# Kernel tuning notes

Hardware: AMD Instinct MI355X
Metric: run time of the kernel (lower is better)

Reference implementation:

```python
import jax, jax.numpy as jnp
import numpy as np

# ---- constants from __init__ ----
DT = 1.0
NX, NY = 192, 192
SRC_X, SRC_Y = 40, 96
PX = jnp.array([160, 160, 160])
PY = jnp.array([48, 96, 144])
PML_N, PML_P, PML_MAX = 20, 4.0, 3.0
C0, C1 = 1.0, 0.9
H = DT * 2.01 / 1.0  # grid spacing


def make_b():
    """PML damping profile b(x,y), [NX, NY]."""
    v = (PML_MAX * np.linspace(0.0, 1.0, PML_N + 1) ** PML_P).astype(np.float32)
    bx = np.zeros((NX, NY), np.float32)
    bx[: PML_N + 1, :] = v[::-1, None]
    bx[NX - PML_N - 1 :, :] = v[:, None]
    by = np.zeros((NX, NY), np.float32)
    by[:, : PML_N + 1] = v[::-1][None, :]
    by[:, NY - PML_N - 1 :] = v[None, :]
    return jnp.asarray(np.sqrt(bx ** 2 + by ** 2))


def _conv3(img, kern):
    # img [B,1,H,W], kern [1,1,3,3], 'same' padding
    return jax.lax.conv_general_dilated(
        img, kern, (1, 1), ((1, 1), (1, 1)),
        dimension_numbers=("NCHW", "OIHW", "NCHW"))


def _proj(x, eta=0.5, beta=100.0):
    return (jnp.tanh(beta * eta) + jnp.tanh(beta * (x - eta))) / (
        jnp.tanh(beta * eta) + jnp.tanh(beta * (1.0 - eta)))


def setup_inputs() -> dict:
    key = jax.random.key(0)
    k1, k2 = jax.random.split(key)
    x = jax.random.normal(k1, (4, 256), dtype=jnp.float32)  # [batch, T]
    rho = jax.random.uniform(k2, (NX, NY), dtype=jnp.float32)
    # clip_pml_rho(): rho[b != 0] = 0 for binarized model (applied at init)
    rho = jnp.where(make_b() != 0, 0.0, rho)
    return {"x": x, "rho": rho}


def reference(x, rho):
    b = make_b()
    lpf_k = jnp.array([[[[0.0, 0.125, 0.0], [0.125, 0.5, 0.125], [0.0, 0.125, 0.0]]]], jnp.float32)
    lap_k = (H ** -2) * jnp.array([[[[0.0, 1.0, 0.0], [1.0, -4.0, 1.0], [0.0, 1.0, 0.0]]]], jnp.float32)
    A1 = 1.0 / (DT ** -2 + b * 0.5 / DT)
    A2 = 2.0 * DT ** -2
    A3 = DT ** -2 - b * 0.5 / DT

    # binarized wave-speed field c(rho): LPF then tanh projection
    lpf_rho = _conv3(rho[None, None], lpf_k)[0, 0]
    c = C0 + (C1 - C0) * _proj(lpf_rho)
    c2 = c * c

    B = x.shape[0]
    y0 = jnp.zeros((B, NX, NY), x.dtype)

    def step(carry, xi):
        y1, y2 = carry
        lap = _conv3(y1[:, None], lap_k)[:, 0]            # [B,NX,NY]
        y = A1 * (A2 * y1 - A3 * y2 + c2 * lap)
        y = y.at[:, SRC_X, SRC_Y].add(xi)                 # source injection
        return (y, y1), y[:, PX, PY]                      # emit probe values [B,P]

    _, probes = jax.lax.scan(step, (y0, y0), x.T)         # probes [T,B,P]

    # integrate_probe_points: sum |y|^2 over time, normalize per batch
    I = jnp.sum(probes ** 2, axis=0)                      # [B,P]
    return I / jnp.sum(I, axis=1, keepdims=True)
```

## Files before the change

### kernel.cpp

```cpp
#include <hip/hip_runtime.h>
#include <math.h>

#define NXY    192
#define CELLS  (NXY*NXY)
#define NBATCH 4
#define NSTEPS 256
#define TCH    16
#define NCHUNK (NSTEPS/TCH)
#define TPB    512
#define NW     8
#define RPL    5
#define OUTR   6
#define NBLKS  256

#define I_OFF   (16*CELLS)
#define FLG_OFF (I_OFF + 64)

typedef float v2f __attribute__((ext_vector_type(2)));

__device__ __forceinline__ float dpp_up1(float v) {
    int r = __builtin_amdgcn_update_dpp(0, __builtin_bit_cast(int, v),
                                        0x138, 0xf, 0xf, true);
    return __builtin_bit_cast(float, r);
}
__device__ __forceinline__ float dpp_dn1(float v) {
    int r = __builtin_amdgcn_update_dpp(0, __builtin_bit_cast(int, v),
                                        0x130, 0xf, 0xf, true);
    return __builtin_bit_cast(float, r);
}

__device__ __forceinline__ float pml_prof(int i) {
    int t;
    if (i <= 20)            t = 20 - i;
    else if (i >= NXY - 21) t = i - (NXY - 21);
    else                    return 0.0f;
    float u  = (float)t * 0.05f;
    float u2 = u * u;
    return 3.0f * u2 * u2;
}

__global__ __launch_bounds__(TPB, 1)
void wave_k(const float* __restrict__ x, const float* __restrict__ rho,
            float* __restrict__ ws, float* __restrict__ out) {
    int blk = ((blockIdx.x & 7) << 5) | (blockIdx.x >> 3);
    int b  = blk / 64;
    int r_ = blk % 64;
    int bi = r_ >> 1, cj = r_ & 1;
    int I0 = OUTR * bi - 17;
    int J0 = 96 * cj - 16;
    int t  = threadIdx.x;
    int w  = t >> 6;
    int l  = t & 63;
    int row0 = I0 + RPL * w;
    int gj   = J0 + 2 * l;

    int* flags = (int*)(ws + FLG_OFF);
    int drt = bi + (t >> 1) - 3;
    int dfi = b * 64 + drt * 2 + (t & 1);
    bool dvalid = (t < 14) && (drt >= 0) && (drt < 32) &&
                  !(drt == bi && (t & 1) == cj);

    __shared__ v2f hb[2][2][NW + 2][64];
    __shared__ float xs[NSTEPS];
    for (int k = t; k < 2 * 2 * (NW + 2) * 64; k += TPB)
        ((v2f*)hb)[k] = (v2f){0.f, 0.f};
    if (t < NSTEPS) xs[t] = x[b * NSTEPS + t];

    bool cok = (gj >= 0 && gj < NXY);

    v2f Ka[RPL], Qa[RPL];
    {
        v2f rv[RPL + 2];
#pragma unroll
        for (int r = 0; r < RPL + 2; r++) {
            int gi = row0 - 1 + r;
            bool ok = cok && gi >= 0 && gi < NXY;
            rv[r] = ok ? *(const v2f*)(rho + gi * NXY + gj) : (v2f){0.f, 0.f};
        }
        const float IH2 = (float)(1.0 / (2.01 * 2.01));
#pragma unroll
        for (int r = 0; r < RPL; r++) {
            int gi = row0 + r;
            v2f rc = rv[r + 1], ru = rv[r], rd = rv[r + 2];
            float lf = dpp_up1(rc.y);
            float rt = dpp_dn1(rc.x);
            float bx = pml_prof(gi);
            v2f K, Q;
            {
                float lpf = 0.5f * rc.x + 0.125f * ((ru.x + rd.x) + (lf + rc.y));
                float p   = 0.5f * (1.0f + tanhf(100.0f * (lpf - 0.5f)));
                float c   = 1.0f - 0.1f * p;
                float by  = pml_prof(gj);
                float bb  = sqrtf(bx * bx + by * by);
                float a1  = 1.0f / (1.0f + 0.5f * bb);
                K.x = a1 * (c * c * IH2);
                Q.x = 1.0f - 2.0f * a1;
            }
            {
                float lpf = 0.5f * rc.y + 0.125f * ((ru.y + rd.y) + (rc.x + rt));
                float p   = 0.5f * (1.0f + tanhf(100.0f * (lpf - 0.5f)));
                float c   = 1.0f - 0.1f * p;
                float by  = pml_prof(gj + 1);
                float bb  = sqrtf(bx * bx + by * by);
                float a1  = 1.0f / (1.0f + 0.5f * bb);
                K.y = a1 * (c * c * IH2);
                Q.y = 1.0f - 2.0f * a1;
            }
            bool ok = cok && gi >= 0 && gi < NXY;
            Ka[r] = ok ? K : (v2f){0.f, 0.f};
            Qa[r] = ok ? Q : (v2f){0.f, 0.f};
        }
    }

    v2f yc[RPL], yp[RPL];
#pragma unroll
    for (int r = 0; r < RPL; r++) { yc[r] = (v2f){0.f, 0.f}; yp[r] = (v2f){0.f, 0.f}; }

    int sr = 40 - I0, sc = 96 - J0;
    bool wave_src = (sr >= RPL * w) && (sr < RPL * w + RPL);
    int src_rl = sr - RPL * w;
    float srcm = (2 * l == sc) ? 1.f : 0.f;

    int pcl = 2 * l + J0;
    bool wave_prb = (bi == 26) && (w == 4);
    const int prb_rl = 1;
    bool is_prb = (cj == 0) ? (pcl == 48) : (pcl == 96 || pcl == 144);
    float prbm = is_prb ? 1.f : 0.f;
    float pacc = 0.f;

    v2f uph, dnh;
    __syncthreads();

#define ROWC(CUR, PRV, rr_, UP, DN, XSV, YN) do {                              \
    v2f cv = CUR[rr_];                                                         \
    float lf0 = dpp_up1(cv.y);                                                 \
    float rt1 = dpp_dn1(cv.x);                                                 \
    v2f h = (v2f){lf0, rt1} + __builtin_shufflevector(cv, cv, 1, 0);           \
    v2f S = ((UP) + (DN)) + h;                                                 \
    YN = cv + Qa[rr_] * (PRV[rr_] - cv) + Ka[rr_] * (S - 4.0f * cv);           \
    if (wave_src && (rr_) == src_rl) YN.x += srcm * (XSV);                     \
    if (wave_prb && (rr_) == prb_rl) { float q = prbm * YN.x; pacc += q * YN.x; } \
} while (0)

#define STEP(CUR, PRV, PH, SIDX) do {                                          \
    v2f y1, y2, y3, t0, t4;                                                    \
    ROWC(CUR, PRV, 1, CUR[0], CUR[2], xv[SIDX], y1);                           \
    ROWC(CUR, PRV, 2, CUR[1], CUR[3], xv[SIDX], y2);                           \
    ROWC(CUR, PRV, 3, CUR[2], CUR[4], xv[SIDX], y3);                           \
    ROWC(CUR, PRV, 0, uph,    CUR[1], xv[SIDX], t0);                           \
    ROWC(CUR, PRV, 4, CUR[3], dnh,    xv[SIDX], t4);                           \
    hb[PH][0][w + 1][l] = t0;                                                  \
    hb[PH][1][w + 1][l] = t4;                                                  \
    PRV[0] = t0; PRV[1] = y1; PRV[2] = y2; PRV[3] = y3; PRV[4] = t4;           \
    __syncthreads();                                                           \
    uph = hb[PH][1][w][l];                                                     \
    dnh = hb[PH][0][w + 2][l];                                                 \
} while (0)

#pragma unroll 1
    for (int chunk = 0; chunk < NCHUNK; chunk++) {
        float xv[TCH];
#pragma unroll
        for (int i = 0; i < TCH; i++) xv[i] = xs[chunk * TCH + i];

        if (chunk) {
            if (dvalid) {
                while (__hip_atomic_load(&flags[dfi], __ATOMIC_RELAXED,
                                         __HIP_MEMORY_SCOPE_AGENT) < chunk) {}
            }
            __syncthreads();

            int pin = chunk & 1;
            const float* curg = ws + ((pin * 2 + 0) * NBATCH + b) * CELLS;
            const float* prvg = ws + ((pin * 2 + 1) * NBATCH + b) * CELLS;
            int  idxr[RPL];
            bool okr[RPL];
#pragma unroll
            for (int r = 0; r < RPL; r++) {
                int gi = row0 + r;
                okr[r]  = cok && gi >= 0 && gi < NXY;
                idxr[r] = okr[r] ? gi * NXY + gj : 0;
            }
            v2f c0, c1, c2, c3, c4, p0, p1, p2, p3, p4;
            asm volatile(
                "global_load_dwordx2 %0, %10, off sc0 sc1\n\t"
                "global_load_dwordx2 %1, %11, off sc0 sc1\n\t"
                "global_load_dwordx2 %2, %12, off sc0 sc1\n\t"
                "global_load_dwordx2 %3, %13, off sc0 sc1\n\t"
                "global_load_dwordx2 %4, %14, off sc0 sc1\n\t"
                "global_load_dwordx2 %5, %15, off sc0 sc1\n\t"
                "global_load_dwordx2 %6, %16, off sc0 sc1\n\t"
                "global_load_dwordx2 %7, %17, off sc0 sc1\n\t"
                "global_load_dwordx2 %8, %18, off sc0 sc1\n\t"
                "global_load_dwordx2 %9, %19, off sc0 sc1\n\t"
                "s_waitcnt vmcnt(0)"
                : "=&v"(c0), "=&v"(c1), "=&v"(c2), "=&v"(c3), "=&v"(c4),
                  "=&v"(p0), "=&v"(p1), "=&v"(p2), "=&v"(p3), "=&v"(p4)
                : "v"(curg + idxr[0]), "v"(curg + idxr[1]), "v"(curg + idxr[2]),
                  "v"(curg + idxr[3]), "v"(curg + idxr[4]),
                  "v"(prvg + idxr[0]), "v"(prvg + idxr[1]), "v"(prvg + idxr[2]),
                  "v"(prvg + idxr[3]), "v"(prvg + idxr[4])
                : "memory");
            yc[0] = okr[0] ? c0 : (v2f){0.f, 0.f};
            yc[1] = okr[1] ? c1 : (v2f){0.f, 0.f};
            yc[2] = okr[2] ? c2 : (v2f){0.f, 0.f};
            yc[3] = okr[3] ? c3 : (v2f){0.f, 0.f};
            yc[4] = okr[4] ? c4 : (v2f){0.f, 0.f};
            yp[0] = okr[0] ? p0 : (v2f){0.f, 0.f};
            yp[1] = okr[1] ? p1 : (v2f){0.f, 0.f};
            yp[2] = okr[2] ? p2 : (v2f){0.f, 0.f};
            yp[3] = okr[3] ? p3 : (v2f){0.f, 0.f};
            yp[4] = okr[4] ? p4 : (v2f){0.f, 0.f};
        }

        hb[0][0][w + 1][l] = yc[0];
        hb[0][1][w + 1][l] = yc[4];
        __syncthreads();
        uph = hb[0][1][w][l];
        dnh = hb[0][0][w + 2][l];

#pragma unroll
        for (int s2 = 0; s2 < TCH / 2; s2++) {
            STEP(yc, yp, 1, 2 * s2);
            STEP(yp, yc, 0, 2 * s2 + 1);
        }

        if (chunk != NCHUNK - 1) {
            int pout = (chunk & 1) ^ 1;
            float* ncurg = ws + ((pout * 2 + 0) * NBATCH + b) * CELLS;
            float* nprvg = ws + ((pout * 2 + 1) * NBATCH + b) * CELLS;
#pragma unroll
            for (int r = 0; r < RPL; r++) {
                int gi = row0 + r;
                if (gi >= OUTR * bi && gi < OUTR * bi + OUTR && l >= 8 && l < 56) {
                    int idx = gi * NXY + gj;
                    asm volatile(
                        "global_store_dwordx2 %0, %2, off sc0 sc1\n\t"
                        "global_store_dwordx2 %1, %3, off sc0 sc1"
                        :: "v"(ncurg + idx), "v"(nprvg + idx),
                           "v"(yc[r]), "v"(yp[r])
                        : "memory");
                }
            }
        } else {
            if (wave_prb && is_prb) {
                float* ip = ws + I_OFF + b * 3 + (pcl / 48 - 1);
                asm volatile("global_store_dword %0, %1, off sc0 sc1"
                             :: "v"(ip), "v"(pacc) : "memory");
            }
        }

        asm volatile("s_waitcnt vmcnt(0)" ::: "memory");
        __syncthreads();
        if (t == 0) {
            __hip_atomic_store(&flags[blk], chunk + 1, __ATOMIC_RELAXED,
                               __HIP_MEMORY_SCOPE_AGENT);
        }
    }
#undef STEP
#undef ROWC

    if (blk == 0) {
        if (t < 8) {
            int pb = (t >> 1) * 64 + 52 + (t & 1);
            while (__hip_atomic_load(&flags[pb], __ATOMIC_RELAXED,
                                     __HIP_MEMORY_SCOPE_AGENT) < NCHUNK) {}
        }
        __syncthreads();
        if (t < 12) {
            const float* I = ws + I_OFF;
            int bb = t / 3;
            float s = 0.f;
#pragma unroll
            for (int k = 0; k < 3; k++)
                s += __hip_atomic_load(I + 3 * bb + k, __ATOMIC_RELAXED,
                                       __HIP_MEMORY_SCOPE_AGENT);
            float num = __hip_atomic_load(I + t, __ATOMIC_RELAXED,
                                          __HIP_MEMORY_SCOPE_AGENT);
            out[t] = num / s;
        }
    }
}

extern "C" void kernel_launch(void* const* d_in, const int* in_sizes, int n_in,
                              void* d_out, int out_size, void* d_ws, size_t ws_size,
                              hipStream_t stream) {
    const float* x   = (const float*)d_in[0];
    const float* rho = (const float*)d_in[1];
    float* ws  = (float*)d_ws;
    float* outp = (float*)d_out;

    hipMemsetAsync((char*)d_ws + I_OFF * sizeof(float), 0,
                   (64 + NBLKS) * sizeof(float), stream);

    wave_k<<<dim3(NBLKS), dim3(TPB), 0, stream>>>(x, rho, ws, outp);
}
```

Measured before the change: 194.4 us.

## Exchange two-row halos per two time steps to halve block barriers

Each wave now keeps a two-row halo on each side and computes two time steps between LDS halo exchanges. The first step redundantly computes 7 rows and the second produces the 5 owned rows, so only one __syncthreads and halo swap happens per pair of steps. The chunk start loads 9 current and 7 previous rows from global memory instead of 5 each. This cuts barrier and LDS latency on the serial time loop in exchange for about 40% more stencil arithmetic per step and higher register use.

```diff
diff --git a/kernel.cpp b/kernel.cpp
--- a/kernel.cpp
+++ b/kernel.cpp
@@ -7,6 +7,7 @@
 #define NSTEPS 256
 #define TCH    16
 #define NCHUNK (NSTEPS/TCH)
+#define NGRP   (TCH/2)
 #define TPB    512
 #define NW     8
 #define RPL    5
@@ -52,6 +53,7 @@
     int w  = t >> 6;
     int l  = t & 63;
     int row0 = I0 + RPL * w;
+    int wr0  = RPL * w;
     int gj   = J0 + 2 * l;
 
     int* flags = (int*)(ws + FLG_OFF);
@@ -60,28 +62,28 @@
     bool dvalid = (t < 14) && (drt >= 0) && (drt < 32) &&
                   !(drt == bi && (t & 1) == cj);
 
-    __shared__ v2f hb[2][2][NW + 2][64];
+    __shared__ v2f hb[2][4][NW + 2][64];
     __shared__ float xs[NSTEPS];
-    for (int k = t; k < 2 * 2 * (NW + 2) * 64; k += TPB)
+    for (int k = t; k < 2 * 4 * (NW + 2) * 64; k += TPB)
         ((v2f*)hb)[k] = (v2f){0.f, 0.f};
     if (t < NSTEPS) xs[t] = x[b * NSTEPS + t];
 
     bool cok = (gj >= 0 && gj < NXY);
 
-    v2f Ka[RPL], Qa[RPL];
+    v2f Ka[7], Qa[7];
     {
-        v2f rv[RPL + 2];
-#pragma unroll
-        for (int r = 0; r < RPL + 2; r++) {
-            int gi = row0 - 1 + r;
+        v2f rv[9];
+#pragma unroll
+        for (int r = 0; r < 9; r++) {
+            int gi = row0 - 2 + r;
             bool ok = cok && gi >= 0 && gi < NXY;
             rv[r] = ok ? *(const v2f*)(rho + gi * NXY + gj) : (v2f){0.f, 0.f};
         }
         const float IH2 = (float)(1.0 / (2.01 * 2.01));
 #pragma unroll
-        for (int r = 0; r < RPL; r++) {
-            int gi = row0 + r;
-            v2f rc = rv[r + 1], ru = rv[r], rd = rv[r + 2];
+        for (int i = 0; i < 7; i++) {
+            int gi = row0 + i - 1;
+            v2f rc = rv[i + 1], ru = rv[i], rd = rv[i + 2];
             float lf = dpp_up1(rc.y);
             float rt = dpp_dn1(rc.x);
             float bx = pml_prof(gi);
@@ -107,54 +109,37 @@
                 Q.y = 1.0f - 2.0f * a1;
             }
             bool ok = cok && gi >= 0 && gi < NXY;
-            Ka[r] = ok ? K : (v2f){0.f, 0.f};
-            Qa[r] = ok ? Q : (v2f){0.f, 0.f};
+            Ka[i] = ok ? K : (v2f){0.f, 0.f};
+            Qa[i] = ok ? Q : (v2f){0.f, 0.f};
         }
     }
 
-    v2f yc[RPL], yp[RPL];
-#pragma unroll
-    for (int r = 0; r < RPL; r++) { yc[r] = (v2f){0.f, 0.f}; yp[r] = (v2f){0.f, 0.f}; }
+    v2f C[9], P[7];
+#pragma unroll
+    for (int i = 0; i < 9; i++) C[i] = (v2f){0.f, 0.f};
+#pragma unroll
+    for (int i = 0; i < 7; i++) P[i] = (v2f){0.f, 0.f};
 
     int sr = 40 - I0, sc = 96 - J0;
-    bool wave_src = (sr >= RPL * w) && (sr < RPL * w + RPL);
-    int src_rl = sr - RPL * w;
     float srcm = (2 * l == sc) ? 1.f : 0.f;
 
     int pcl = 2 * l + J0;
     bool wave_prb = (bi == 26) && (w == 4);
-    const int prb_rl = 1;
     bool is_prb = (cj == 0) ? (pcl == 48) : (pcl == 96 || pcl == 144);
     float prbm = is_prb ? 1.f : 0.f;
     float pacc = 0.f;
 
-    v2f uph, dnh;
     __syncthreads();
 
-#define ROWC(CUR, PRV, rr_, UP, DN, XSV, YN) do {                              \
-    v2f cv = CUR[rr_];                                                         \
+#define ROWC2(cv_, pv_, K_, Q_, up_, dn_, XSV, WROW, YN) do {                  \
+    v2f cv = (cv_);                                                            \
     float lf0 = dpp_up1(cv.y);                                                 \
     float rt1 = dpp_dn1(cv.x);                                                 \
     v2f h = (v2f){lf0, rt1} + __builtin_shufflevector(cv, cv, 1, 0);           \
-    v2f S = ((UP) + (DN)) + h;                                                 \
-    YN = cv + Qa[rr_] * (PRV[rr_] - cv) + Ka[rr_] * (S - 4.0f * cv);           \
-    if (wave_src && (rr_) == src_rl) YN.x += srcm * (XSV);                     \
-    if (wave_prb && (rr_) == prb_rl) { float q = prbm * YN.x; pacc += q * YN.x; } \
-} while (0)
-
-#define STEP(CUR, PRV, PH, SIDX) do {                                          \
-    v2f y1, y2, y3, t0, t4;                                                    \
-    ROWC(CUR, PRV, 1, CUR[0], CUR[2], xv[SIDX], y1);                           \
-    ROWC(CUR, PRV, 2, CUR[1], CUR[3], xv[SIDX], y2);                           \
-    ROWC(CUR, PRV, 3, CUR[2], CUR[4], xv[SIDX], y3);                           \
-    ROWC(CUR, PRV, 0, uph,    CUR[1], xv[SIDX], t0);                           \
-    ROWC(CUR, PRV, 4, CUR[3], dnh,    xv[SIDX], t4);                           \
-    hb[PH][0][w + 1][l] = t0;                                                  \
-    hb[PH][1][w + 1][l] = t4;                                                  \
-    PRV[0] = t0; PRV[1] = y1; PRV[2] = y2; PRV[3] = y3; PRV[4] = t4;           \
-    __syncthreads();                                                           \
-    uph = hb[PH][1][w][l];                                                     \
-    dnh = hb[PH][0][w + 2][l];                                                 \
+    v2f S = ((up_) + (dn_)) + h;                                               \
+    YN = cv + (Q_) * ((pv_) - cv) + (K_) * (S - 4.0f * cv);                    \
+    if ((WROW) == sr) YN.x += srcm * (XSV);                                    \
+    if (wave_prb && (WROW) == 21) { float q = prbm * YN.x; pacc += q * YN.x; } \
 } while (0)
 
 #pragma unroll 1
@@ -173,56 +158,66 @@
             int pin = chunk & 1;
             const float* curg = ws + ((pin * 2 + 0) * NBATCH + b) * CELLS;
             const float* prvg = ws + ((pin * 2 + 1) * NBATCH + b) * CELLS;
-            int  idxr[RPL];
-            bool okr[RPL];
-#pragma unroll
-            for (int r = 0; r < RPL; r++) {
-                int gi = row0 + r;
-                okr[r]  = cok && gi >= 0 && gi < NXY;
-                idxr[r] = okr[r] ? gi * NXY + gj : 0;
-            }
-            v2f c0, c1, c2, c3, c4, p0, p1, p2, p3, p4;
-            asm volatile(
-                "global_load_dwordx2 %0, %10, off sc0 sc1\n\t"
-                "global_load_dwordx2 %1, %11, off sc0 sc1\n\t"
-                "global_load_dwordx2 %2, %12, off sc0 sc1\n\t"
-                "global_load_dwordx2 %3, %13, off sc0 sc1\n\t"
-                "global_load_dwordx2 %4, %14, off sc0 sc1\n\t"
-                "global_load_dwordx2 %5, %15, off sc0 sc1\n\t"
-                "global_load_dwordx2 %6, %16, off sc0 sc1\n\t"
-                "global_load_dwordx2 %7, %17, off sc0 sc1\n\t"
-                "global_load_dwordx2 %8, %18, off sc0 sc1\n\t"
-                "global_load_dwordx2 %9, %19, off sc0 sc1\n\t"
-                "s_waitcnt vmcnt(0)"
-                : "=&v"(c0), "=&v"(c1), "=&v"(c2), "=&v"(c3), "=&v"(c4),
-                  "=&v"(p0), "=&v"(p1), "=&v"(p2), "=&v"(p3), "=&v"(p4)
-                : "v"(curg + idxr[0]), "v"(curg + idxr[1]), "v"(curg + idxr[2]),
-                  "v"(curg + idxr[3]), "v"(curg + idxr[4]),
-                  "v"(prvg + idxr[0]), "v"(prvg + idxr[1]), "v"(prvg + idxr[2]),
-                  "v"(prvg + idxr[3]), "v"(prvg + idxr[4])
-                : "memory");
-            yc[0] = okr[0] ? c0 : (v2f){0.f, 0.f};
-            yc[1] = okr[1] ? c1 : (v2f){0.f, 0.f};
-            yc[2] = okr[2] ? c2 : (v2f){0.f, 0.f};
-            yc[3] = okr[3] ? c3 : (v2f){0.f, 0.f};
-            yc[4] = okr[4] ? c4 : (v2f){0.f, 0.f};
-            yp[0] = okr[0] ? p0 : (v2f){0.f, 0.f};
-            yp[1] = okr[1] ? p1 : (v2f){0.f, 0.f};
-            yp[2] = okr[2] ? p2 : (v2f){0.f, 0.f};
-            yp[3] = okr[3] ? p3 : (v2f){0.f, 0.f};
-            yp[4] = okr[4] ? p4 : (v2f){0.f, 0.f};
-        }
-
-        hb[0][0][w + 1][l] = yc[0];
-        hb[0][1][w + 1][l] = yc[4];
-        __syncthreads();
-        uph = hb[0][1][w][l];
-        dnh = hb[0][0][w + 2][l];
-
-#pragma unroll
-        for (int s2 = 0; s2 < TCH / 2; s2++) {
-            STEP(yc, yp, 1, 2 * s2);
-            STEP(yp, yc, 0, 2 * s2 + 1);
+            const float* ac[9]; const float* ap[7];
+            bool okc[9], okp[7];
+#pragma unroll
+            for (int i = 0; i < 9; i++) {
+                int gi = row0 + i - 2;
+                okc[i] = cok && gi >= 0 && gi < NXY;
+                ac[i]  = curg + (okc[i] ? gi * NXY + gj : 0);
+            }
+#pragma unroll
+            for (int i = 0; i < 7; i++) {
+                int gi = row0 + i - 1;
+                okp[i] = cok && gi >= 0 && gi < NXY;
+                ap[i]  = prvg + (okp[i] ? gi * NXY + gj : 0);
+            }
+            v2f lc[9], lp[7];
+#pragma unroll
+            for (int i = 0; i < 9; i++)
+                asm volatile("global_load_dwordx2 %0, %1, off sc0 sc1"
+                             : "=&v"(lc[i]) : "v"(ac[i]));
+#pragma unroll
+            for (int i = 0; i < 7; i++)
+                asm volatile("global_load_dwordx2 %0, %1, off sc0 sc1"
+                             : "=&v"(lp[i]) : "v"(ap[i]));
+            asm volatile("s_waitcnt vmcnt(0)" ::: "memory");
+            __builtin_amdgcn_sched_barrier(0);
+#pragma unroll
+            for (int i = 0; i < 9; i++) C[i] = okc[i] ? lc[i] : (v2f){0.f, 0.f};
+#pragma unroll
+            for (int i = 0; i < 7; i++) P[i] = okp[i] ? lp[i] : (v2f){0.f, 0.f};
+        }
+
+        v2f A[7], Bv[5];
+#pragma unroll
+        for (int g = 0; g < NGRP; g++) {
+            float xA = xv[2 * g], xB = xv[2 * g + 1];
+#pragma unroll
+            for (int i = 0; i < 7; i++)
+                ROWC2(C[i + 1], P[i], Ka[i], Qa[i], C[i], C[i + 2],
+                      xA, wr0 + i - 1, A[i]);
+#pragma unroll
+            for (int j = 0; j < 5; j++)
+                ROWC2(A[j + 1], C[j + 2], Ka[j + 1], Qa[j + 1], A[j], A[j + 2],
+                      xB, wr0 + j, Bv[j]);
+
+            if (g != NGRP - 1) {
+                int ph = g & 1;
+                hb[ph][0][w + 1][l] = Bv[0];
+                hb[ph][1][w + 1][l] = Bv[1];
+                hb[ph][2][w + 1][l] = Bv[3];
+                hb[ph][3][w + 1][l] = Bv[4];
+                __syncthreads();
+                C[0] = hb[ph][2][w][l];
+                C[1] = hb[ph][3][w][l];
+                C[7] = hb[ph][0][w + 2][l];
+                C[8] = hb[ph][1][w + 2][l];
+                C[2] = Bv[0]; C[3] = Bv[1]; C[4] = Bv[2];
+                C[5] = Bv[3]; C[6] = Bv[4];
+#pragma unroll
+                for (int i = 0; i < 7; i++) P[i] = A[i];
+            }
         }
 
         if (chunk != NCHUNK - 1) {
@@ -230,15 +225,15 @@
             float* ncurg = ws + ((pout * 2 + 0) * NBATCH + b) * CELLS;
             float* nprvg = ws + ((pout * 2 + 1) * NBATCH + b) * CELLS;
 #pragma unroll
-            for (int r = 0; r < RPL; r++) {
-                int gi = row0 + r;
+            for (int j = 0; j < 5; j++) {
+                int gi = row0 + j;
                 if (gi >= OUTR * bi && gi < OUTR * bi + OUTR && l >= 8 && l < 56) {
                     int idx = gi * NXY + gj;
                     asm volatile(
                         "global_store_dwordx2 %0, %2, off sc0 sc1\n\t"
                         "global_store_dwordx2 %1, %3, off sc0 sc1"
                         :: "v"(ncurg + idx), "v"(nprvg + idx),
-                           "v"(yc[r]), "v"(yp[r])
+                           "v"(Bv[j]), "v"(A[j + 1])
                         : "memory");
                 }
             }
@@ -257,8 +252,7 @@
                                __HIP_MEMORY_SCOPE_AGENT);
         }
     }
-#undef STEP
-#undef ROWC
+#undef ROWC2
 
     if (blk == 0) {
         if (t < 8) {
```

New measurement: 195.0 us. Within noise of the previous version (+0.3%).
